# Performance work log

Hardware: AMD Instinct MI355X
Metric: run time of the kernel (lower is better)

Reference implementation:

```python
import jax, jax.numpy as jnp
import numpy as np

B, H, W, D = 16, 56, 56, 384
NH, WS, SH = 12, 7, 3
HD = D // NH
N = WS * WS
nW = (H // WS) * (W // WS)
L = H * W

def _rel_pos_index():
    c = np.stack(np.meshgrid(np.arange(WS), np.arange(WS), indexing='ij')).reshape(2, -1)
    r = (c[:, :, None] - c[:, None, :]).transpose(1, 2, 0)
    r[:, :, 0] += WS - 1
    r[:, :, 1] += WS - 1
    r[:, :, 0] *= 2 * WS - 1
    return r.sum(-1)  # (N, N) int indices into bias table

RPI = _rel_pos_index()

def _attn_mask():
    img = np.zeros((H, W))
    cnt = 0
    sl = (slice(0, H - WS), slice(H - WS, H - SH), slice(H - SH, None))
    for hs in sl:
        for ws in sl:
            img[hs, ws] = cnt
            cnt += 1
    mw = img.reshape(H // WS, WS, W // WS, WS).transpose(0, 2, 1, 3).reshape(-1, N)
    am = mw[:, None, :] - mw[:, :, None]
    return np.where(am != 0, -100.0, 0.0).astype(np.float32)  # (nW, N, N)

AM = jnp.asarray(_attn_mask())

def _ln(x, g, b):
    m = jnp.mean(x, -1, keepdims=True)
    v = jnp.mean((x - m) ** 2, -1, keepdims=True)
    return (x - m) * jax.lax.rsqrt(v + 1e-5) * g + b

def _fwd(x, norm1_g, norm1_b, qkv_w, qkv_b, rpb, proj_w, proj_b, norm2_g, norm2_b,
         fc1_w, fc1_b, fc2_w, fc2_b, expand_w, exnorm_g, exnorm_b):
    def blk(x, i, shifted):
        sc = x
        h = _ln(x, norm1_g[i], norm1_b[i]).reshape(B, H, W, D)
        if shifted:
            h = jnp.roll(h, (-SH, -SH), axis=(1, 2))
        # window partition: (B*nW, N, D)
        xw = h.reshape(B, H // WS, WS, W // WS, WS, D).transpose(0, 1, 3, 2, 4, 5).reshape(-1, N, D)
        qkv = (xw @ qkv_w[i] + qkv_b[i]).reshape(-1, N, 3, NH, HD).transpose(2, 0, 3, 1, 4)
        q, k, v = qkv[0] * HD ** -0.5, qkv[1], qkv[2]
        bias = rpb[i][RPI].transpose(2, 0, 1)  # (NH, N, N)
        attn = jnp.einsum('bhid,bhjd->bhij', q, k) + bias[None]
        if shifted:
            attn = (attn.reshape(B, nW, NH, N, N) + AM[None, :, None]).reshape(-1, NH, N, N)
        attn = jax.nn.softmax(attn, axis=-1)
        o = jnp.einsum('bhij,bhjd->bhid', attn, v).transpose(0, 2, 1, 3).reshape(-1, N, D)
        o = o @ proj_w[i] + proj_b[i]
        # window reverse: (B, H, W, D)
        o = o.reshape(B, H // WS, W // WS, WS, WS, D).transpose(0, 1, 3, 2, 4, 5).reshape(B, H, W, D)
        if shifted:
            o = jnp.roll(o, (SH, SH), axis=(1, 2))
        x = sc + o.reshape(B, L, D)
        h2 = _ln(x, norm2_g[i], norm2_b[i])
        h2 = jax.nn.gelu(h2 @ fc1_w[i] + fc1_b[i], approximate=False) @ fc2_w[i] + fc2_b[i]
        return x + h2

    x = blk(x, 0, False)  # W-MSA
    x = blk(x, 1, True)   # SW-MSA
    # PatchExpand: dim -> 2*dim, pixel-shuffle 2x2, norm(dim/2)
    xe = (x @ expand_w).reshape(B, H, W, 2, 2, D // 2)
    xe = xe.transpose(0, 1, 3, 2, 4, 5).reshape(B, 4 * L, D // 2)
    return _ln(xe, exnorm_g, exnorm_b)

def setup_inputs() -> dict:
    ks = jax.random.split(jax.random.key(0), 8)
    r = lambda k, s: jax.random.normal(k, s, jnp.float32) * 0.02
    return {
        'x': jax.random.normal(ks[0], (B, L, D), jnp.float32),
        'norm1_g': jnp.ones((2, D)), 'norm1_b': jnp.zeros((2, D)),
        'qkv_w': r(ks[1], (2, D, 3 * D)), 'qkv_b': jnp.zeros((2, 3 * D)),
        'rpb': r(ks[2], (2, (2 * WS - 1) ** 2, NH)),
        'proj_w': r(ks[3], (2, D, D)), 'proj_b': jnp.zeros((2, D)),
        'norm2_g': jnp.ones((2, D)), 'norm2_b': jnp.zeros((2, D)),
        'fc1_w': r(ks[4], (2, D, 4 * D)), 'fc1_b': jnp.zeros((2, 4 * D)),
        'fc2_w': r(ks[5], (2, 4 * D, D)), 'fc2_b': jnp.zeros((2, D)),
        'expand_w': r(ks[6], (D, 2 * D)),
        'exnorm_g': jnp.ones((D // 2,)), 'exnorm_b': jnp.zeros((D // 2,)),
    }

def reference(x, norm1_g, norm1_b, qkv_w, qkv_b, rpb, proj_w, proj_b, norm2_g, norm2_b,
              fc1_w, fc1_b, fc2_w, fc2_b, expand_w, exnorm_g, exnorm_b):
    return _fwd(x, norm1_g, norm1_b, qkv_w, qkv_b, rpb, proj_w, proj_b, norm2_g, norm2_b,
                fc1_w, fc1_b, fc2_w, fc2_b, expand_w, exnorm_g, exnorm_b)
```

## Files before the change

kernel.cpp:

```cpp
#include <hip/hip_runtime.h>
#include <cstdint>
#include <cstddef>

typedef unsigned short u16;
typedef unsigned int u32;
typedef __attribute__((ext_vector_type(8))) short bf16x8;
typedef __attribute__((ext_vector_type(4))) float f32x4;

__device__ __forceinline__ float bf2f(u32 u) {
  union { u32 i; float f; } c; c.i = u << 16; return c.f;
}
__device__ __forceinline__ u16 f2bf(float f) {
  union { float f; u32 i; } c; c.f = f;
  u32 r = c.i + 0x7fffu + ((c.i >> 16) & 1u);
  return (u16)(r >> 16);
}

__device__ __forceinline__ float gelu_f(float x) {
  float z = 0.70710678118654752f * x;
  float az = fabsf(z);
  float d = __builtin_fmaf(0.3275911f, az, 1.f);
  float t = __builtin_amdgcn_rcpf(d);
  float p = t * (0.254829592f + t * (-0.284496736f + t * (1.421413741f +
            t * (-1.453152027f + t * 1.061405429f))));
  float e = __expf(-az * az);
  float er = __builtin_fmaf(-p, e, 1.f);
  er = copysignf(er, z);
  return 0.5f * x * (1.f + er);
}

__device__ __forceinline__ int srcrow_map(int m, int shifted) {
  int w = m / 49, n = m - w * 49;
  int b = w >> 6, wi = w & 63;
  int wy = wi >> 3, wx = wi & 7;
  int ty = n / 7, tx = n - ty * 7;
  int h = wy * 7 + ty, x = wx * 7 + tx;
  if (shifted) { h += 3; if (h >= 56) h -= 56; x += 3; if (x >= 56) x -= 56; }
  return b * 3136 + h * 56 + x;
}

__global__ void detect_kernel(const u32* __restrict__ x, int* __restrict__ flag) {
  int t = threadIdx.x;
  int c = 0;
  for (int i = t; i < 1024; i += 256) {
    u32 e = (x[i] >> 7) & 0xFFu;
    c += (e >= 100 && e <= 130) ? 1 : 0;
  }
#pragma unroll
  for (int m = 1; m < 64; m <<= 1) c += __shfl_xor(c, m, 64);
  __shared__ int part[4];
  if ((t & 63) == 0) part[t >> 6] = c;
  __syncthreads();
  if (t == 0) flag[0] = (part[0] + part[1] + part[2] + part[3] > 700) ? 1 : 0;
}

__global__ void convert_kernel(const void* __restrict__ in, u16* __restrict__ out,
                               int n4, const int* __restrict__ flag) {
  int i = blockIdx.x * 256 + threadIdx.x;
  if (i >= n4) return;
  if (flag[0]) {
    ((uint2*)out)[i] = ((const uint2*)in)[i];
  } else {
    float4 v = ((const float4*)in)[i];
    uint2 r;
    r.x = (u32)f2bf(v.x) | ((u32)f2bf(v.y) << 16);
    r.y = (u32)f2bf(v.z) | ((u32)f2bf(v.w) << 16);
    ((uint2*)out)[i] = r;
  }
}

__global__ void transpose_kernel(const void* __restrict__ in, u16* __restrict__ out,
                                 int R, int C, int total, const int* __restrict__ flag) {
  int i = blockIdx.x * 256 + threadIdx.x;
  if (i >= total) return;
  int rc = R * C;
  int bb = i / rc, rem = i - bb * rc;
  int c = rem / R, r = rem - c * R;
  size_t s = (size_t)bb * rc + (size_t)r * C + c;
  out[i] = flag[0] ? ((const u16*)in)[s] : f2bf(((const float*)in)[s]);
}

__global__ __launch_bounds__(256)
void ln384_kernel(const u16* __restrict__ in, const u16* __restrict__ g,
                  const u16* __restrict__ b, u16* __restrict__ out) {
  int row = blockIdx.x * 4 + (threadIdx.x >> 6);
  int lane = threadIdx.x & 63;
  const u32* p = (const u32*)(in + (size_t)row * 384);
  float x[6]; float sum = 0.f, sq = 0.f;
#pragma unroll
  for (int j = 0; j < 3; ++j) {
    u32 u = p[lane + 64 * j];
    float a0 = bf2f(u & 0xffff), a1 = bf2f(u >> 16);
    x[2 * j] = a0; x[2 * j + 1] = a1;
    sum += a0 + a1; sq += a0 * a0 + a1 * a1;
  }
#pragma unroll
  for (int m = 1; m < 64; m <<= 1) { sum += __shfl_xor(sum, m, 64); sq += __shfl_xor(sq, m, 64); }
  float mean = sum * (1.f / 384.f);
  float var = sq * (1.f / 384.f) - mean * mean;
  float rstd = rsqrtf(var + 1e-5f);
  u32* op = (u32*)(out + (size_t)row * 384);
  const u32* g32 = (const u32*)g; const u32* b32 = (const u32*)b;
#pragma unroll
  for (int j = 0; j < 3; ++j) {
    int c = lane + 64 * j;
    u32 gg = g32[c], bb = b32[c];
    float y0 = (x[2 * j] - mean) * rstd * bf2f(gg & 0xffff) + bf2f(bb & 0xffff);
    float y1 = (x[2 * j + 1] - mean) * rstd * bf2f(gg >> 16) + bf2f(bb >> 16);
    op[c] = (u32)f2bf(y0) | ((u32)f2bf(y1) << 16);
  }
}

__global__ __launch_bounds__(256)
void lnfinal_kernel(const u16* __restrict__ in, const u16* __restrict__ g,
                    const u16* __restrict__ b, void* __restrict__ outv,
                    const int* __restrict__ flag) {
  int row = blockIdx.x * 8 + (threadIdx.x >> 5);
  int s = threadIdx.x & 31;
  int fl = flag[0];
  int bb = row / 12544, rem = row - bb * 12544;
  int hh = rem / 112, wp = rem - hh * 112;
  int h = hh >> 1, a = hh & 1, w = wp >> 1, c2 = wp & 1;
  const u32* p = (const u32*)(in + ((size_t)(bb * 3136 + h * 56 + w)) * 768 + (a * 2 + c2) * 192);
  float x[6]; float sum = 0.f, sq = 0.f;
#pragma unroll
  for (int j = 0; j < 3; ++j) {
    u32 u = p[s + 32 * j];
    float a0 = bf2f(u & 0xffff), a1 = bf2f(u >> 16);
    x[2 * j] = a0; x[2 * j + 1] = a1;
    sum += a0 + a1; sq += a0 * a0 + a1 * a1;
  }
#pragma unroll
  for (int m = 1; m < 32; m <<= 1) { sum += __shfl_xor(sum, m, 32); sq += __shfl_xor(sq, m, 32); }
  float mean = sum * (1.f / 192.f);
  float var = sq * (1.f / 192.f) - mean * mean;
  float rstd = rsqrtf(var + 1e-5f);
  const u32* g32 = (const u32*)g; const u32* b32 = (const u32*)b;
#pragma unroll
  for (int j = 0; j < 3; ++j) {
    int c = s + 32 * j;
    u32 gg = g32[c], bv = b32[c];
    float y0 = (x[2 * j] - mean) * rstd * bf2f(gg & 0xffff) + bf2f(bv & 0xffff);
    float y1 = (x[2 * j + 1] - mean) * rstd * bf2f(gg >> 16) + bf2f(bv >> 16);
    if (fl) {
      u32* op = (u32*)((u16*)outv + (size_t)row * 192);
      op[c] = (u32)f2bf(y0) | ((u32)f2bf(y1) << 16);
    } else {
      float2* op = (float2*)((float*)outv + (size_t)row * 192);
      float2 v; v.x = y0; v.y = y1;
      op[c] = v;
    }
  }
}

template <int MODE>
__global__ __launch_bounds__(256, 2)
void gemm_kernel(const u16* __restrict__ A, const u16* __restrict__ Bt,
                 const u16* __restrict__ bias, const u16* __restrict__ resid,
                 u16* __restrict__ C, int N, int K, int shifted, int nn) {
  __shared__ __attribute__((aligned(16))) char smem[32768];

  const int t = threadIdx.x;
  const int lane = t & 63;
  const int wave = t >> 6;

  const int wgid = (blockIdx.x & 7) * ((int)gridDim.x >> 3) + (blockIdx.x >> 3);
  const int mblk = wgid / nn, nblk = wgid - mblk * nn;

  const u16* aptr[2]; const u16* bptr[2];
  char* ldsa[2]; char* ldsb[2];
#pragma unroll
  for (int i = 0; i < 2; ++i) {
    int c = t + i * 256;
    int r = c >> 2, off8 = (c & 3) * 8;
    int gr = mblk * 128 + r;
    int src = (MODE == 0) ? srcrow_map(gr, shifted) : gr;
    aptr[i] = A + (size_t)src * K + off8;
    int gn = nblk * 128 + r;
    bptr[i] = Bt + (size_t)gn * K + off8;
    ldsa[i] = smem + c * 16;
    ldsb[i] = smem + 8192 + c * 16;
  }

  f32x4 acc[4][4];
#pragma unroll
  for (int i = 0; i < 4; ++i)
#pragma unroll
    for (int j = 0; j < 4; ++j) { f32x4 z = {0.f, 0.f, 0.f, 0.f}; acc[i][j] = z; }

  const int quad = lane >> 4, l15 = lane & 15;
  const int wm = (wave >> 1) * 64, wn = (wave & 1) * 64;

  auto stage = [&](int b) {
#pragma unroll
    for (int i = 0; i < 2; ++i) {
      __builtin_amdgcn_global_load_lds((const void*)aptr[i], (void*)(ldsa[i] + b * 16384), 16, 0, 0);
      __builtin_amdgcn_global_load_lds((const void*)bptr[i], (void*)(ldsb[i] + b * 16384), 16, 0, 0);
      aptr[i] += 32; bptr[i] += 32;
    }
  };
  auto compute = [&](int b) {
    const u16* As = (const u16*)(smem + b * 16384);
    const u16* Bs = (const u16*)(smem + b * 16384 + 8192);
    bf16x8 af[4], bfv[4];
#pragma unroll
    for (int mt = 0; mt < 4; ++mt)
      af[mt] = *(const bf16x8*)(As + (wm + mt * 16 + l15) * 32 + quad * 8);
#pragma unroll
    for (int nt = 0; nt < 4; ++nt)
      bfv[nt] = *(const bf16x8*)(Bs + (wn + nt * 16 + l15) * 32 + quad * 8);
#pragma unroll
    for (int mt = 0; mt < 4; ++mt)
#pragma unroll
      for (int nt = 0; nt < 4; ++nt)
        acc[mt][nt] = __builtin_amdgcn_mfma_f32_16x16x32_bf16(af[mt], bfv[nt], acc[mt][nt], 0, 0, 0);
  };

  const int ktiles = K >> 5;
  stage(0);
  __syncthreads();
  int cur = 0;
  for (int kt = 0; kt < ktiles - 1; ++kt) {
    stage(cur ^ 1);
    compute(cur);
    __syncthreads();
    cur ^= 1;
  }
  compute(cur);

  size_t rowoff[4][4];
#pragma unroll
  for (int mt = 0; mt < 4; ++mt) {
#pragma unroll
    for (int r = 0; r < 4; ++r) {
      int rr = mblk * 128 + wm + mt * 16 + quad * 4 + r;
      if (MODE == 0) {
        int w49 = rr / 49, n49 = rr - w49 * 49;
        rowoff[mt][r] = (size_t)(w49 * 18816 + n49 * 32);
      } else if (MODE == 1) {
        rowoff[mt][r] = (size_t)srcrow_map(rr, shifted) * 384;
      } else {
        rowoff[mt][r] = (size_t)rr * (size_t)N;
      }
    }
  }
#pragma unroll
  for (int nt = 0; nt < 4; ++nt) {
    const int cb = nblk * 128 + wn + nt * 16;
    const int col = cb + l15;
    const float bcol = (MODE == 4) ? 0.f : bf2f(bias[col]);
    size_t ntoff; float qsc = 1.f;
    if (MODE == 0) {
      int part = cb / 384;
      int cw = cb - part * 384;
      int head = cw >> 5, hdb = cw & 31;
      qsc = (part == 0) ? 0.17677669529663689f : 1.f;
      ntoff = (size_t)part * 19267584 + (size_t)head * 1568 + (size_t)(hdb + l15);
    } else {
      ntoff = (size_t)col;
    }
#pragma unroll
    for (int mt = 0; mt < 4; ++mt) {
#pragma unroll
      for (int r = 0; r < 4; ++r) {
        float v = acc[mt][nt][r];
        size_t o = rowoff[mt][r] + ntoff;
        if (MODE == 0) {
          C[o] = f2bf((v + bcol) * qsc);
        } else if (MODE == 1) {
          C[o] = f2bf(v + bcol + bf2f(resid[o]));
        } else if (MODE == 2) {
          C[o] = f2bf(gelu_f(v + bcol));
        } else if (MODE == 3) {
          C[o] = f2bf(v + bcol + bf2f(resid[o]));
        } else {
          C[o] = f2bf(v);
        }
      }
    }
  }
}

__global__ void biastab_kernel(const u16* __restrict__ rpb, float* __restrict__ bt, int shifted) {
  int idx = blockIdx.x * 256 + threadIdx.x;
  if (idx >= 4 * 12 * 2401) return;
  int ij = idx % 2401, ch = idx / 2401;
  int head = ch % 12, cls = ch / 12;
  int i = ij / 49, j = ij % 49;
  int iy = i / 7, ix = i - iy * 7, jy = j / 7, jx = j - jy * 7;
  int rp = (iy - jy + 6) * 13 + (ix - jx + 6);
  float v = bf2f(rpb[rp * 12 + head]);
  if (shifted) {
    int clsy = cls >> 1, clsx = cls & 1;
    int regi = (clsy ? (iy < 4 ? 1 : 2) : 0) * 3 + (clsx ? (ix < 4 ? 1 : 2) : 0);
    int regj = (clsy ? (jy < 4 ? 1 : 2) : 0) * 3 + (clsx ? (jx < 4 ? 1 : 2) : 0);
    if (regi != regj) v -= 100.f;
  }
  bt[idx] = v;
}

__global__ __launch_bounds__(256, 3)
void attn_mfma_kernel(const u16* __restrict__ qkv, const float* __restrict__ bt,
                      u16* __restrict__ o) {
  __shared__ __attribute__((aligned(16))) char pbuf[4][8192];
  const int wave = threadIdx.x >> 6;
  const int lane = threadIdx.x & 63;
  const int quad = lane >> 4, l15 = lane & 15;
  const int blk = blockIdx.x * 4 + wave;
  const int w = blk / 12, head = blk - w * 12;
  const int wi = w & 63;
  const int cls = (((wi >> 3) == 7) ? 2 : 0) + (((wi & 7) == 7) ? 1 : 0);
  const float* btw = bt + (size_t)(cls * 12 + head) * 2401;
  char* pw = &pbuf[wave][0];

  const size_t base = (size_t)blk * 1568;
  const u16* qp = qkv + base;
  const u16* kp = qkv + 19267584 + base;
  const u16* vp = qkv + 2 * 19267584 + base;

  bf16x8 qf[4], kf[4];
#pragma unroll
  for (int mi = 0; mi < 4; ++mi)
    qf[mi] = *(const bf16x8*)(qp + (size_t)(mi * 16 + l15) * 32 + quad * 8);
#pragma unroll
  for (int nj = 0; nj < 4; ++nj)
    kf[nj] = *(const bf16x8*)(kp + (size_t)(nj * 16 + l15) * 32 + quad * 8);

  bf16x8 vf[2][2];
#pragma unroll
  for (int kk = 0; kk < 2; ++kk)
#pragma unroll
    for (int n2 = 0; n2 < 2; ++n2) {
      bf16x8 tv;
#pragma unroll
      for (int j = 0; j < 8; ++j) {
        int key = kk * 32 + quad * 8 + j;
        u16 raw = vp[(size_t)key * 32 + n2 * 16 + l15];
        tv[j] = (key < 49) ? (short)raw : (short)0;
      }
      vf[kk][n2] = tv;
    }

  f32x4 s[4][4];
#pragma unroll
  for (int mi = 0; mi < 4; ++mi)
#pragma unroll
    for (int nj = 0; nj < 4; ++nj) { f32x4 z = {0.f, 0.f, 0.f, 0.f}; s[mi][nj] = z; }
#pragma unroll
  for (int mi = 0; mi < 4; ++mi)
#pragma unroll
    for (int nj = 0; nj < 4; ++nj)
      s[mi][nj] = __builtin_amdgcn_mfma_f32_16x16x32_bf16(qf[mi], kf[nj], s[mi][nj], 0, 0, 0);

  const bool c3ok = (l15 == 0);
#pragma unroll
  for (int mi = 0; mi < 4; ++mi) {
#pragma unroll
    for (int r = 0; r < 4; ++r) {
      int i = mi * 16 + quad * 4 + r;
      const float* brow = btw + i * 49;
      float v0 = s[mi][0][r] + brow[l15];
      float v1 = s[mi][1][r] + brow[l15 + 16];
      float v2 = s[mi][2][r] + brow[l15 + 32];
      float v3 = c3ok ? (s[mi][3][r] + brow[48]) : -1e30f;
      float mx = fmaxf(fmaxf(v0, v1), fmaxf(v2, v3));
#pragma unroll
      for (int t = 1; t < 16; t <<= 1) mx = fmaxf(mx, __shfl_xor(mx, t, 64));
      float e0 = __expf(v0 - mx), e1 = __expf(v1 - mx);
      float e2 = __expf(v2 - mx), e3 = __expf(v3 - mx);
      float ls = e0 + e1 + e2 + e3;
#pragma unroll
      for (int t = 1; t < 16; t <<= 1) ls += __shfl_xor(ls, t, 64);
      float inv = 1.f / ls;
      u32 sw = (u32)((i & 7) << 4);
      *(u16*)(pw + (((u32)(i * 128 + l15 * 2)) ^ sw)) = f2bf(e0 * inv);
      *(u16*)(pw + (((u32)(i * 128 + (l15 + 16) * 2)) ^ sw)) = f2bf(e1 * inv);
      *(u16*)(pw + (((u32)(i * 128 + (l15 + 32) * 2)) ^ sw)) = f2bf(e2 * inv);
      *(u16*)(pw + (((u32)(i * 128 + (l15 + 48) * 2)) ^ sw)) = f2bf(e3 * inv);
    }
  }

  asm volatile("s_waitcnt lgkmcnt(0)" ::: "memory");
  __builtin_amdgcn_sched_barrier(0);

  f32x4 oacc[4][2];
#pragma unroll
  for (int mi = 0; mi < 4; ++mi)
#pragma unroll
    for (int n2 = 0; n2 < 2; ++n2) { f32x4 z = {0.f, 0.f, 0.f, 0.f}; oacc[mi][n2] = z; }
#pragma unroll
  for (int mi = 0; mi < 4; ++mi) {
#pragma unroll
    for (int kk = 0; kk < 2; ++kk) {
      int arow = mi * 16 + l15;
      u32 ab = ((u32)(arow * 128 + (kk * 32 + quad * 8) * 2)) ^ ((u32)((arow & 7) << 4));
      bf16x8 pf = *(const bf16x8*)(pw + ab);
#pragma unroll
      for (int n2 = 0; n2 < 2; ++n2)
        oacc[mi][n2] = __builtin_amdgcn_mfma_f32_16x16x32_bf16(pf, vf[kk][n2], oacc[mi][n2], 0, 0, 0);
    }
  }

#pragma unroll
  for (int mi = 0; mi < 4; ++mi)
#pragma unroll
    for (int r = 0; r < 4; ++r) {
      int row = mi * 16 + quad * 4 + r;
      if (row < 49) {
        u16* orow = o + ((size_t)(w * 49 + row)) * 384 + head * 32;
        orow[l15] = f2bf(oacc[mi][0][r]);
        orow[16 + l15] = f2bf(oacc[mi][1][r]);
      }
    }
}

extern "C" void kernel_launch(void* const* d_in, const int* in_sizes, int n_in,
                              void* d_out, int out_size, void* d_ws, size_t ws_size,
                              hipStream_t stream) {
  char* ws = (char*)d_ws;
  u16* wsA  = (u16*)ws;
  u16* wsS  = (u16*)(ws + 154140672);
  u16* wsB  = (u16*)(ws + 192675840);
  u16* wsT  = (u16*)(ws + 231211008);
  u16* wsP  = (u16*)(ws + 238878720);
  int* flag = (int*)(ws + 238907568);
  float* bt = (float*)(ws + 115736576);

  u16* qkvT  = wsT;
  u16* projT = qkvT + 2 * 442368;
  u16* fc1T  = projT + 2 * 147456;
  u16* fc2T  = fc1T + 2 * 589824;
  u16* expT  = fc2T + 2 * 589824;

  u16* p_n1g  = wsP + 0;
  u16* p_n1b  = wsP + 768;
  u16* p_qkvb = wsP + 1536;
  u16* p_rpb  = wsP + 3840;
  u16* p_prjb = wsP + 7896;
  u16* p_n2g  = wsP + 8664;
  u16* p_n2b  = wsP + 9432;
  u16* p_fc1b = wsP + 10200;
  u16* p_fc2b = wsP + 13272;
  u16* p_exg  = wsP + 14040;
  u16* p_exb  = wsP + 14232;

  detect_kernel<<<1, 256, 0, stream>>>((const u32*)d_in[0], flag);

  convert_kernel<<<(19267584 / 4 + 255) / 256, 256, 0, stream>>>(d_in[0], wsS, 19267584 / 4, flag);
  auto cv = [&](const void* src, u16* dst, int n) {
    convert_kernel<<<(n / 4 + 255) / 256, 256, 0, stream>>>(src, dst, n / 4, flag);
  };
  cv(d_in[1],  p_n1g, 768);   cv(d_in[2],  p_n1b, 768);
  cv(d_in[4],  p_qkvb, 2304); cv(d_in[5],  p_rpb, 4056);
  cv(d_in[7],  p_prjb, 768);  cv(d_in[8],  p_n2g, 768);
  cv(d_in[9],  p_n2b, 768);   cv(d_in[11], p_fc1b, 3072);
  cv(d_in[13], p_fc2b, 768);  cv(d_in[15], p_exg, 192);
  cv(d_in[16], p_exb, 192);

  {
    int tot;
    tot = 2 * 384 * 1152; transpose_kernel<<<(tot + 255) / 256, 256, 0, stream>>>(d_in[3],  qkvT, 384, 1152, tot, flag);
    tot = 2 * 384 * 384;  transpose_kernel<<<(tot + 255) / 256, 256, 0, stream>>>(d_in[6],  projT, 384, 384,  tot, flag);
    tot = 2 * 384 * 1536; transpose_kernel<<<(tot + 255) / 256, 256, 0, stream>>>(d_in[10], fc1T, 384, 1536, tot, flag);
    tot = 2 * 1536 * 384; transpose_kernel<<<(tot + 255) / 256, 256, 0, stream>>>(d_in[12], fc2T, 1536, 384, tot, flag);
    tot = 384 * 768;      transpose_kernel<<<(tot + 255) / 256, 256, 0, stream>>>(d_in[14], expT, 384, 768,  tot, flag);
  }

  for (int i = 0; i < 2; ++i) {
    int shifted = i;
    biastab_kernel<<<451, 256, 0, stream>>>(p_rpb + i * 2028, bt, shifted);
    ln384_kernel<<<12544, 256, 0, stream>>>(wsS, p_n1g + i * 384, p_n1b + i * 384, wsB);
    gemm_kernel<0><<<3528, 256, 0, stream>>>(wsB, qkvT + i * 442368, p_qkvb + i * 1152,
                                             nullptr, wsA, 1152, 384, shifted, 9);
    attn_mfma_kernel<<<3072, 256, 0, stream>>>(wsA, bt, wsB);
    gemm_kernel<1><<<1176, 256, 0, stream>>>(wsB, projT + i * 147456, p_prjb + i * 384,
                                             wsS, wsS, 384, 384, shifted, 3);
    ln384_kernel<<<12544, 256, 0, stream>>>(wsS, p_n2g + i * 384, p_n2b + i * 384, wsB);
    gemm_kernel<2><<<4704, 256, 0, stream>>>(wsB, fc1T + i * 589824, p_fc1b + i * 1536,
                                             nullptr, wsA, 1536, 384, 0, 12);
    gemm_kernel<3><<<1176, 256, 0, stream>>>(wsA, fc2T + i * 589824, p_fc2b + i * 384,
                                             wsS, wsS, 384, 1536, 0, 3);
  }

  gemm_kernel<4><<<2352, 256, 0, stream>>>(wsS, expT, nullptr, nullptr, wsA, 768, 384, 0, 6);
  lnfinal_kernel<<<25088, 256, 0, stream>>>(wsA, p_exg, p_exb, d_out, flag);
}
```

Baseline: 1.161 ms.

## Triple-buffer GEMM LDS tiles with partial vmcnt waits and reorder epilogue

```diff
diff --git a/kernel.cpp b/kernel.cpp
--- a/kernel.cpp
+++ b/kernel.cpp
@@ -158,7 +158,7 @@
 void gemm_kernel(const u16* __restrict__ A, const u16* __restrict__ Bt,
                  const u16* __restrict__ bias, const u16* __restrict__ resid,
                  u16* __restrict__ C, int N, int K, int shifted, int nn) {
-  __shared__ __attribute__((aligned(16))) char smem[32768];
+  __shared__ __attribute__((aligned(16))) char smem[49152];
 
   const int t = threadIdx.x;
   const int lane = t & 63;
@@ -218,15 +218,27 @@
 
   const int ktiles = K >> 5;
   stage(0);
-  __syncthreads();
-  int cur = 0;
-  for (int kt = 0; kt < ktiles - 1; ++kt) {
-    stage(cur ^ 1);
-    compute(cur);
-    __syncthreads();
-    cur ^= 1;
-  }
-  compute(cur);
+  stage(1);
+  asm volatile("s_waitcnt vmcnt(4)" ::: "memory");
+  __builtin_amdgcn_s_barrier();
+  __builtin_amdgcn_sched_barrier(0);
+  int bcur = 0, bstage = 2;
+  for (int kt = 0; kt < ktiles; ++kt) {
+    const bool more2 = (kt + 2 < ktiles);
+    if (more2) stage(bstage);
+    compute(bcur);
+    if (more2) {
+      asm volatile("s_waitcnt vmcnt(4)" ::: "memory");
+      __builtin_amdgcn_s_barrier();
+      __builtin_amdgcn_sched_barrier(0);
+    } else if (kt + 1 < ktiles) {
+      asm volatile("s_waitcnt vmcnt(0)" ::: "memory");
+      __builtin_amdgcn_s_barrier();
+      __builtin_amdgcn_sched_barrier(0);
+    }
+    bcur = (bcur == 2) ? 0 : bcur + 1;
+    bstage = (bstage == 2) ? 0 : bstage + 1;
+  }
 
   size_t rowoff[4][4];
 #pragma unroll
@@ -244,35 +256,40 @@
       }
     }
   }
+  size_t ntoff[4]; float bcolv[4]; float qscv[4];
 #pragma unroll
   for (int nt = 0; nt < 4; ++nt) {
     const int cb = nblk * 128 + wn + nt * 16;
     const int col = cb + l15;
-    const float bcol = (MODE == 4) ? 0.f : bf2f(bias[col]);
-    size_t ntoff; float qsc = 1.f;
+    bcolv[nt] = (MODE == 4) ? 0.f : bf2f(bias[col]);
+    qscv[nt] = 1.f;
     if (MODE == 0) {
       int part = cb / 384;
       int cw = cb - part * 384;
       int head = cw >> 5, hdb = cw & 31;
-      qsc = (part == 0) ? 0.17677669529663689f : 1.f;
-      ntoff = (size_t)part * 19267584 + (size_t)head * 1568 + (size_t)(hdb + l15);
+      qscv[nt] = (part == 0) ? 0.17677669529663689f : 1.f;
+      ntoff[nt] = (size_t)part * 19267584 + (size_t)head * 1568 + (size_t)(hdb + l15);
     } else {
-      ntoff = (size_t)col;
-    }
-#pragma unroll
-    for (int mt = 0; mt < 4; ++mt) {
-#pragma unroll
-      for (int r = 0; r < 4; ++r) {
+      ntoff[nt] = (size_t)col;
+    }
+  }
+#pragma unroll
+  for (int mt = 0; mt < 4; ++mt) {
+#pragma unroll
+    for (int r = 0; r < 4; ++r) {
+      const size_t ro = rowoff[mt][r];
+#pragma unroll
+      for (int nt = 0; nt < 4; ++nt) {
         float v = acc[mt][nt][r];
-        size_t o = rowoff[mt][r] + ntoff;
+        size_t o = ro + ntoff[nt];
         if (MODE == 0) {
-          C[o] = f2bf((v + bcol) * qsc);
+          C[o] = f2bf((v + bcolv[nt]) * qscv[nt]);
         } else if (MODE == 1) {
-          C[o] = f2bf(v + bcol + bf2f(resid[o]));
+          C[o] = f2bf(v + bcolv[nt] + bf2f(resid[o]));
         } else if (MODE == 2) {
-          C[o] = f2bf(gelu_f(v + bcol));
+          C[o] = f2bf(gelu_f(v + bcolv[nt]));
         } else if (MODE == 3) {
-          C[o] = f2bf(v + bcol + bf2f(resid[o]));
+          C[o] = f2bf(v + bcolv[nt] + bf2f(resid[o]));
         } else {
           C[o] = f2bf(v);
         }
```

Result: faster. 1.078 ms (-7.2%).
